# Performance work log

Measured on AMD Instinct MI355X. Metric: run time of the kernel, lower is better.

## Reference

```python
import jax, jax.numpy as jnp
import numpy as np

B, M, N_STYLE, K, F = 4, 8192, 8192, 8, 288


def _graphconv(x, src, dst, W, b, num_nodes):
    # DGL GraphConv, norm='both': h_v = (sum_{u->v} x_u * d_out(u)^-1/2) * d_in(v)^-1/2 @ W + b
    ones = jnp.ones(src.shape[0], x.dtype)
    deg_out = jnp.clip(jax.ops.segment_sum(ones, src, num_segments=num_nodes), 1.0)
    deg_in = jnp.clip(jax.ops.segment_sum(ones, dst, num_segments=num_nodes), 1.0)
    h = x * (deg_out ** -0.5)[:, None]                      # [N, F] src-normalized
    agg = jax.ops.segment_sum(h[src], dst, num_segments=num_nodes)  # gather+scatter-add
    agg = agg * (deg_in ** -0.5)[:, None]
    return agg @ W + b


def setup_inputs() -> dict:
    key = jax.random.key(0)
    ks = jax.random.split(key, 8)
    return {
        "feat_c": jax.random.normal(ks[0], (B, M, F), jnp.float32),
        "feat_s": jax.random.normal(ks[1], (B, N_STYLE, F), jnp.float32),
        "idx_k1": jax.random.randint(ks[2], (B, M, K), 0, N_STYLE, dtype=jnp.int32),
        "idx_k2": jax.random.randint(ks[3], (B, M, K), 0, M, dtype=jnp.int32),
        "W1": jax.random.normal(ks[4], (F, F), jnp.float32) * (1.0 / np.sqrt(F)),
        "b1": jnp.zeros((F,), jnp.float32),
        "W2": jax.random.normal(ks[5], (F, F), jnp.float32) * (1.0 / np.sqrt(F)),
        "b2": jnp.zeros((F,), jnp.float32),
    }


def reference(feat_c, feat_s, idx_k1, idx_k2, W1, b1, W2, b2):
    b, m, f = feat_c.shape
    n = feat_s.shape[1]
    k = idx_k1.shape[2]
    num_nodes = m + n
    # idx_v: range(m).view(1,m,1).expand(2,m,k).view(-1)
    idx_v = jnp.tile(jnp.repeat(jnp.arange(m, dtype=jnp.int32), k), 2)  # [2*m*k]
    # idx_u: cat((idx_k2, idx_k1 + m), dim=1).view(b, -1)
    idx_u = jnp.concatenate([idx_k2, idx_k1 + m], axis=1).reshape(b, -1)  # [b, 2*m*k]
    feat = jnp.concatenate([feat_c, feat_s], axis=1)  # [b, m+n, f]

    def per_graph(x, src):
        h = _graphconv(x, src, idx_v, W1, b1, num_nodes)
        h = jax.nn.relu(h)
        h = _graphconv(h, src, idx_v, W2, b2, num_nodes)
        return h[:m]  # [m, f]

    return jax.vmap(per_graph)(feat, idx_u)  # [b, m, f]
```

## Files before the change

kernel.cpp:

```cpp
#include <hip/hip_runtime.h>

#define B 4
#define M 8192
#define NSTY 8192
#define KNB 8
#define F 288
#define NT (M + NSTY)
#define BM (B * M)
#define SEGL (M * F)

typedef __attribute__((ext_vector_type(8))) short short8;
typedef __attribute__((ext_vector_type(4))) float floatx4;
typedef __attribute__((ext_vector_type(2))) float floatx2;

__device__ __forceinline__ float u2f(unsigned int u) {
    union { unsigned int u; float f; } c; c.u = u; return c.f;
}
__device__ __forceinline__ unsigned short f2b(float x) {
    union { float f; unsigned int u; } c; c.f = x;
    unsigned int r = c.u + 0x7FFFu + ((c.u >> 16) & 1u);
    return (unsigned short)(r >> 16);
}
__device__ __forceinline__ floatx2 bpair(unsigned int p) {
    floatx2 r;
    r.x = u2f(p << 16);
    r.y = u2f(p & 0xFFFF0000u);
    return r;
}
__device__ __forceinline__ void gload_lds16(const void* g, void* l) {
    __builtin_amdgcn_global_load_lds(
        (const __attribute__((address_space(1))) unsigned int*)g,
        (__attribute__((address_space(3))) unsigned int*)l, 16, 0, 0);
}

#define PREP_DEG_BLKS 4
#define PREP_CVT_BLKS 576
#define PREP_PKW_BLKS 162
__global__ __launch_bounds__(1024) void prep_kernel(
                            const int* __restrict__ idx_k1, const int* __restrict__ idx_k2,
                            int* __restrict__ deg,
                            const float* __restrict__ fc, const float* __restrict__ fs,
                            unsigned short* __restrict__ fb,
                            const float* __restrict__ W1, const float* __restrict__ W2,
                            unsigned short* __restrict__ Wp1, unsigned short* __restrict__ Wp2) {
    int blk = blockIdx.x;
    int tid = threadIdx.x;
    if (blk < PREP_DEG_BLKS) {
        __shared__ int h[NT];
        for (int i = tid; i < NT; i += 1024) h[i] = 0;
        __syncthreads();
        int b = blk;
        const int4* p2 = (const int4*)(idx_k2 + (size_t)b * M * KNB);
        const int4* p1 = (const int4*)(idx_k1 + (size_t)b * M * KNB);
        #pragma unroll 2
        for (int i = tid; i < (M * KNB) / 4; i += 1024) {
            int4 v = p2[i];
            atomicAdd(&h[v.x], 1); atomicAdd(&h[v.y], 1);
            atomicAdd(&h[v.z], 1); atomicAdd(&h[v.w], 1);
        }
        #pragma unroll 2
        for (int i = tid; i < (M * KNB) / 4; i += 1024) {
            int4 v = p1[i];
            atomicAdd(&h[M + v.x], 1); atomicAdd(&h[M + v.y], 1);
            atomicAdd(&h[M + v.z], 1); atomicAdd(&h[M + v.w], 1);
        }
        __syncthreads();
        int4* dst = (int4*)(deg + (size_t)b * NT);
        const int4* hs = (const int4*)h;
        for (int i = tid; i < NT / 4; i += 1024) dst[i] = hs[i];
    } else if (blk < PREP_DEG_BLKS + PREP_CVT_BLKS) {
        int cb = blk - PREP_DEG_BLKS;
        int seg = cb / 72;
        int bis = cb - seg * 72;
        int b = seg >> 1, sty = seg & 1;
        const float* src0 = (sty ? fs : fc) + (size_t)b * SEGL;
        unsigned short* dst0 = fb + (size_t)b * 2 * SEGL + (size_t)sty * SEGL;
        unsigned int e0 = (unsigned int)bis * 32768u + (unsigned int)tid * 8u;
        float4 x[8];
        #pragma unroll
        for (int j = 0; j < 4; ++j) {
            const float* s = src0 + e0 + j * 8192u;
            x[2 * j]     = *(const float4*)s;
            x[2 * j + 1] = *(const float4*)(s + 4);
        }
        #pragma unroll
        for (int j = 0; j < 4; ++j) {
            uint4 o;
            o.x = (unsigned int)f2b(x[2*j].x)   | ((unsigned int)f2b(x[2*j].y)   << 16);
            o.y = (unsigned int)f2b(x[2*j].z)   | ((unsigned int)f2b(x[2*j].w)   << 16);
            o.z = (unsigned int)f2b(x[2*j+1].x) | ((unsigned int)f2b(x[2*j+1].y) << 16);
            o.w = (unsigned int)f2b(x[2*j+1].z) | ((unsigned int)f2b(x[2*j+1].w) << 16);
            *(uint4*)(dst0 + e0 + j * 8192u) = o;
        }
    } else {
        int t = (blk - PREP_DEG_BLKS - PREP_CVT_BLKS) * 1024 + tid;
        if (t >= 2 * F * F) return;
        int half = t >= F * F;
        int tt = t - half * F * F;
        int k = tt / F, n = tt - k * F;
        const float* W = half ? W2 : W1;
        unsigned short* Wp = half ? Wp2 : Wp1;
        Wp[((size_t)(k >> 3) * F + n) * 8 + (k & 7)] = f2b(W[tt]);
    }
}

template<int LAYER>
__global__ __launch_bounds__(256) void agg_kernel(
        const unsigned short* __restrict__ src_tbl,
        const int* __restrict__ idx_k1, const int* __restrict__ idx_k2,
        const int* __restrict__ deg, const float* __restrict__ b1,
        unsigned short* __restrict__ aggb) {
    const int NK = (LAYER == 1) ? 16 : 8;
    int tid = threadIdx.x, wid = tid >> 6, lane = tid & 63;
    int blk = blockIdx.x;
    int rx = blk & 7;
    int b = rx >> 1;
    int sub = (blk >> 3) * 2 + (rx & 1);
    int rbase = sub * 16 + wid * 4;

    int i4 = lane >> 4, e = lane & 15;
    size_t eb = ((size_t)b * M + rbase + i4) * KNB;
    int u;
    if (e < 8) u = idx_k2[eb + e];
    else       u = M + idx_k1[eb + e - 8];
    int dg = deg[b * NT + u];
    float w = rsqrtf((float)(dg < 1 ? 1 : dg));
    float wst = (e >= 8) ? w : 0.f;
    unsigned int uoff = (unsigned int)u * (unsigned int)(F * 2);

    float bb[8];
    if (LAYER == 2 && lane < 36) {
        float4 t0 = *(const float4*)(b1 + 8 * lane);
        float4 t1 = *(const float4*)(b1 + 8 * lane + 4);
        bb[0]=fmaxf(t0.x,0.f); bb[1]=fmaxf(t0.y,0.f); bb[2]=fmaxf(t0.z,0.f); bb[3]=fmaxf(t0.w,0.f);
        bb[4]=fmaxf(t1.x,0.f); bb[5]=fmaxf(t1.y,0.f); bb[6]=fmaxf(t1.z,0.f); bb[7]=fmaxf(t1.w,0.f);
    }

    const char* baseb = (const char*)(src_tbl + (size_t)b * (LAYER == 1 ? NT : M) * F);
    unsigned int lane16 = (unsigned int)lane * 16u;
    unsigned short* dbase = aggb + ((size_t)b * M + rbase) * F;

    #pragma unroll
    for (int i = 0; i < 4; ++i) {
        unsigned int off[NK];
        #pragma unroll
        for (int k = 0; k < NK; ++k)
            off[k] = (unsigned int)__shfl((int)uoff, i * 16 + k) + lane16;
        uint4 v[NK];
        if (lane < 36) {
            #pragma unroll
            for (int k = 0; k < NK; ++k) v[k] = *(const uint4*)(baseb + off[k]);
        }

        floatx2 acc[4];
        if (LAYER == 2) {
            float S = 0.f;
            #pragma unroll
            for (int j = 8; j < 16; ++j) S += __shfl(wst, i * 16 + j);
            #pragma unroll
            for (int j = 0; j < 4; ++j) { acc[j].x = bb[2*j] * S; acc[j].y = bb[2*j+1] * S; }
        } else {
            #pragma unroll
            for (int j = 0; j < 4; ++j) acc[j] = (floatx2){0.f, 0.f};
        }

        #pragma unroll
        for (int k = 0; k < NK; ++k) {
            float wk = __shfl(w, i * 16 + k);
            floatx2 wk2 = {wk, wk};
            acc[0] += wk2 * bpair(v[k].x);
            acc[1] += wk2 * bpair(v[k].y);
            acc[2] += wk2 * bpair(v[k].z);
            acc[3] += wk2 * bpair(v[k].w);
        }

        if (lane < 36) {
            uint4 o;
            o.x = (unsigned int)f2b(acc[0].x*0.25f) | ((unsigned int)f2b(acc[0].y*0.25f) << 16);
            o.y = (unsigned int)f2b(acc[1].x*0.25f) | ((unsigned int)f2b(acc[1].y*0.25f) << 16);
            o.z = (unsigned int)f2b(acc[2].x*0.25f) | ((unsigned int)f2b(acc[2].y*0.25f) << 16);
            o.w = (unsigned int)f2b(acc[3].x*0.25f) | ((unsigned int)f2b(acc[3].y*0.25f) << 16);
            *(uint4*)(dbase + (size_t)i * F + 8 * lane) = o;
        }
    }
}

template<int RELU, int OUTBF16>
__global__ __launch_bounds__(256, 2) void gemm_kernel(
        const unsigned short* __restrict__ A,
        const unsigned short* __restrict__ Wp,
        const float* __restrict__ bias,
        void* __restrict__ Cout) {
    __shared__ __align__(16) unsigned short sA[64 * F];
    __shared__ __align__(16) unsigned short sB[2][4 * F * 8];
    int tid = threadIdx.x;
    int wid = tid >> 6, lane = tid & 63;
    int wm = wid & 1, wn = wid >> 1;
    int quad = lane >> 4, r16 = lane & 15;
    int blk = blockIdx.x;
    int rx = blk & 7;
    int b = rx >> 1;
    int sub = (blk >> 3) * 2 + (rx & 1);
    int row0 = b * M + sub * 64;

    const unsigned short* Ab = A + (size_t)row0 * F;
    #pragma unroll
    for (int rr = 0; rr < 9; ++rr)
        gload_lds16(Ab + (rr * 256 + tid) * 8, &sA[(rr * 256 + tid) * 8]);
    if (tid < 128) {
        #pragma unroll
        for (int rr = 0; rr < 9; ++rr)
            gload_lds16(Wp + (rr * 128 + tid) * 8, &sB[0][(rr * 128 + tid) * 8]);
    }

    floatx4 acc[9][2];
    #pragma unroll
    for (int ct = 0; ct < 9; ++ct)
        #pragma unroll
        for (int rt = 0; rt < 2; ++rt)
            acc[ct][rt] = (floatx4){0.f, 0.f, 0.f, 0.f};

    __syncthreads();

    for (int s = 0; s < 9; ++s) {
        if (s < 8 && tid < 128) {
            const unsigned short* src = Wp + (size_t)(s + 1) * 4 * F * 8;
            unsigned short* dstb = sB[(s + 1) & 1];
            #pragma unroll
            for (int rr = 0; rr < 9; ++rr)
                gload_lds16(src + (rr * 128 + tid) * 8, dstb + (rr * 128 + tid) * 8);
        }
        short8 a0 = *(const short8*)&sA[(wm * 32 + r16) * F + s * 32 + quad * 8];
        short8 a1 = *(const short8*)&sA[(wm * 32 + 16 + r16) * F + s * 32 + quad * 8];
        const unsigned short* bbp = &sB[s & 1][(quad * F + wn * 144 + r16) * 8];
        #pragma unroll
        for (int ct = 0; ct < 9; ++ct) {
            short8 bf = *(const short8*)(bbp + ct * 128);
            acc[ct][0] = __builtin_amdgcn_mfma_f32_16x16x32_bf16(a0, bf, acc[ct][0], 0, 0, 0);
            acc[ct][1] = __builtin_amdgcn_mfma_f32_16x16x32_bf16(a1, bf, acc[ct][1], 0, 0, 0);
        }
        __syncthreads();
    }

    #pragma unroll
    for (int ct = 0; ct < 9; ++ct) {
        int col = wn * 144 + ct * 16 + r16;
        float bc = bias[col];
        #pragma unroll
        for (int rt = 0; rt < 2; ++rt) {
            #pragma unroll
            for (int rg = 0; rg < 4; ++rg) {
                float v = acc[ct][rt][rg] + bc;
                if (RELU) v = fmaxf(v, 0.f);
                int grow = row0 + wm * 32 + quad * 4 + rt * 16 + rg;
                if (OUTBF16) ((unsigned short*)Cout)[(size_t)grow * F + col] = f2b(v);
                else         ((float*)Cout)[(size_t)grow * F + col] = v;
            }
        }
    }
}

extern "C" void kernel_launch(void* const* d_in, const int* in_sizes, int n_in,
                              void* d_out, int out_size, void* d_ws, size_t ws_size,
                              hipStream_t stream) {
    const float* feat_c = (const float*)d_in[0];
    const float* feat_s = (const float*)d_in[1];
    const int*   idx_k1 = (const int*)d_in[2];
    const int*   idx_k2 = (const int*)d_in[3];
    const float* W1     = (const float*)d_in[4];
    const float* b1     = (const float*)d_in[5];
    const float* W2     = (const float*)d_in[6];
    const float* b2     = (const float*)d_in[7];

    char* ws = (char*)d_ws;
    int*            deg  = (int*)ws;
    unsigned short* Wp1  = (unsigned short*)(ws + 262144);
    unsigned short* Wp2  = (unsigned short*)(ws + 262144 + 165888);
    unsigned short* aggb = (unsigned short*)(ws + 262144 + 2 * 165888);

    unsigned short* featb = (unsigned short*)d_out;
    unsigned short* h1b   = (unsigned short*)d_out;
    float*          out   = (float*)d_out;

    prep_kernel<<<PREP_DEG_BLKS + PREP_CVT_BLKS + PREP_PKW_BLKS, 1024, 0, stream>>>(
        idx_k1, idx_k2, deg, feat_c, feat_s, featb, W1, W2, Wp1, Wp2);

    agg_kernel<1><<<BM / 16, 256, 0, stream>>>(featb, idx_k1, idx_k2, deg, b1, aggb);
    gemm_kernel<1, 1><<<BM / 64, 256, 0, stream>>>(aggb, Wp1, b1, (void*)h1b);

    agg_kernel<2><<<BM / 16, 256, 0, stream>>>(h1b, idx_k1, idx_k2, deg, b1, aggb);
    gemm_kernel<0, 0><<<BM / 64, 256, 0, stream>>>(aggb, Wp2, b2, (void*)out);
}
```

Measured before the change: 219.9 us.

## Fuse neighbor aggregation into GEMM kernel via shared-memory A tile

Merges the gather/aggregate kernel and the bf16 MFMA GEMM into one 512-thread kernel per layer. Aggregated rows go straight into the LDS A tile instead of round-tripping through a global buffer. This removes two launches and the write and re-read of the aggregated matrix. In exchange, blocks are larger (8 waves, each computing a 16-row MFMA slice), the weight prefetch is issued before the gather, and h1 now lives in workspace instead of the output buffer.

```diff
diff --git a/kernel.cpp b/kernel.cpp
--- a/kernel.cpp
+++ b/kernel.cpp
@@ -105,139 +105,127 @@
 }
 
 template<int LAYER>
-__global__ __launch_bounds__(256) void agg_kernel(
+__global__ __launch_bounds__(512, 4) void fused_kernel(
         const unsigned short* __restrict__ src_tbl,
         const int* __restrict__ idx_k1, const int* __restrict__ idx_k2,
-        const int* __restrict__ deg, const float* __restrict__ b1,
-        unsigned short* __restrict__ aggb) {
+        const int* __restrict__ deg,
+        const float* __restrict__ bprev,
+        const unsigned short* __restrict__ Wp,
+        const float* __restrict__ bias,
+        void* __restrict__ Cout) {
     const int NK = (LAYER == 1) ? 16 : 8;
-    int tid = threadIdx.x, wid = tid >> 6, lane = tid & 63;
+    __shared__ __align__(16) unsigned short sA[64 * F];
+    __shared__ __align__(16) unsigned short sB[2][4 * F * 8];
+
+    int tid = threadIdx.x;
+    int wid = tid >> 6, lane = tid & 63;
     int blk = blockIdx.x;
     int rx = blk & 7;
     int b = rx >> 1;
     int sub = (blk >> 3) * 2 + (rx & 1);
-    int rbase = sub * 16 + wid * 4;
+    int rloc = sub * 64;
+    int row0 = b * M + rloc;
+
+    if (tid < 128) {
+        #pragma unroll
+        for (int rr = 0; rr < 9; ++rr)
+            gload_lds16(Wp + (rr * 128 + tid) * 8, &sB[0][(rr * 128 + tid) * 8]);
+    }
 
     int i4 = lane >> 4, e = lane & 15;
-    size_t eb = ((size_t)b * M + rbase + i4) * KNB;
-    int u;
-    if (e < 8) u = idx_k2[eb + e];
-    else       u = M + idx_k1[eb + e - 8];
-    int dg = deg[b * NT + u];
-    float w = rsqrtf((float)(dg < 1 ? 1 : dg));
-    float wst = (e >= 8) ? w : 0.f;
-    unsigned int uoff = (unsigned int)u * (unsigned int)(F * 2);
+    const char* baseb = (const char*)(src_tbl + (size_t)b * (size_t)(LAYER == 1 ? NT : M) * F);
+    unsigned int lane16 = (unsigned int)lane * 16u;
 
     float bb[8];
     if (LAYER == 2 && lane < 36) {
-        float4 t0 = *(const float4*)(b1 + 8 * lane);
-        float4 t1 = *(const float4*)(b1 + 8 * lane + 4);
+        float4 t0 = *(const float4*)(bprev + 8 * lane);
+        float4 t1 = *(const float4*)(bprev + 8 * lane + 4);
         bb[0]=fmaxf(t0.x,0.f); bb[1]=fmaxf(t0.y,0.f); bb[2]=fmaxf(t0.z,0.f); bb[3]=fmaxf(t0.w,0.f);
         bb[4]=fmaxf(t1.x,0.f); bb[5]=fmaxf(t1.y,0.f); bb[6]=fmaxf(t1.z,0.f); bb[7]=fmaxf(t1.w,0.f);
     }
 
-    const char* baseb = (const char*)(src_tbl + (size_t)b * (LAYER == 1 ? NT : M) * F);
-    unsigned int lane16 = (unsigned int)lane * 16u;
-    unsigned short* dbase = aggb + ((size_t)b * M + rbase) * F;
-
     #pragma unroll
-    for (int i = 0; i < 4; ++i) {
-        unsigned int off[NK];
-        #pragma unroll
-        for (int k = 0; k < NK; ++k)
-            off[k] = (unsigned int)__shfl((int)uoff, i * 16 + k) + lane16;
-        uint4 v[NK];
-        if (lane < 36) {
+    for (int p = 0; p < 2; ++p) {
+        int rb = wid * 8 + p * 4;
+        size_t eb = ((size_t)b * M + rloc + rb + i4) * KNB;
+        int u;
+        if (e < 8) u = idx_k2[eb + e];
+        else       u = M + idx_k1[eb + e - 8];
+        int dg = deg[b * NT + u];
+        float w = rsqrtf((float)(dg < 1 ? 1 : dg));
+        float wst = (e >= 8) ? w : 0.f;
+        unsigned int uoff = (unsigned int)u * (unsigned int)(F * 2);
+
+        #pragma unroll
+        for (int i = 0; i < 4; ++i) {
+            floatx2 acc[4];
+            if (LAYER == 2) {
+                float S = 0.f;
+                #pragma unroll
+                for (int j = 8; j < 16; ++j) S += __shfl(wst, i * 16 + j);
+                #pragma unroll
+                for (int j = 0; j < 4; ++j) { acc[j].x = bb[2*j] * S; acc[j].y = bb[2*j+1] * S; }
+            } else {
+                #pragma unroll
+                for (int j = 0; j < 4; ++j) acc[j] = (floatx2){0.f, 0.f};
+            }
+
             #pragma unroll
-            for (int k = 0; k < NK; ++k) v[k] = *(const uint4*)(baseb + off[k]);
-        }
-
-        floatx2 acc[4];
-        if (LAYER == 2) {
-            float S = 0.f;
-            #pragma unroll
-            for (int j = 8; j < 16; ++j) S += __shfl(wst, i * 16 + j);
-            #pragma unroll
-            for (int j = 0; j < 4; ++j) { acc[j].x = bb[2*j] * S; acc[j].y = bb[2*j+1] * S; }
-        } else {
-            #pragma unroll
-            for (int j = 0; j < 4; ++j) acc[j] = (floatx2){0.f, 0.f};
-        }
-
-        #pragma unroll
-        for (int k = 0; k < NK; ++k) {
-            float wk = __shfl(w, i * 16 + k);
-            floatx2 wk2 = {wk, wk};
-            acc[0] += wk2 * bpair(v[k].x);
-            acc[1] += wk2 * bpair(v[k].y);
-            acc[2] += wk2 * bpair(v[k].z);
-            acc[3] += wk2 * bpair(v[k].w);
-        }
-
-        if (lane < 36) {
-            uint4 o;
-            o.x = (unsigned int)f2b(acc[0].x*0.25f) | ((unsigned int)f2b(acc[0].y*0.25f) << 16);
-            o.y = (unsigned int)f2b(acc[1].x*0.25f) | ((unsigned int)f2b(acc[1].y*0.25f) << 16);
-            o.z = (unsigned int)f2b(acc[2].x*0.25f) | ((unsigned int)f2b(acc[2].y*0.25f) << 16);
-            o.w = (unsigned int)f2b(acc[3].x*0.25f) | ((unsigned int)f2b(acc[3].y*0.25f) << 16);
-            *(uint4*)(dbase + (size_t)i * F + 8 * lane) = o;
-        }
-    }
-}
-
-template<int RELU, int OUTBF16>
-__global__ __launch_bounds__(256, 2) void gemm_kernel(
-        const unsigned short* __restrict__ A,
-        const unsigned short* __restrict__ Wp,
-        const float* __restrict__ bias,
-        void* __restrict__ Cout) {
-    __shared__ __align__(16) unsigned short sA[64 * F];
-    __shared__ __align__(16) unsigned short sB[2][4 * F * 8];
-    int tid = threadIdx.x;
-    int wid = tid >> 6, lane = tid & 63;
-    int wm = wid & 1, wn = wid >> 1;
+            for (int c = 0; c < NK / 8; ++c) {
+                unsigned int off[8];
+                #pragma unroll
+                for (int k = 0; k < 8; ++k)
+                    off[k] = (unsigned int)__shfl((int)uoff, i * 16 + c * 8 + k) + lane16;
+                uint4 v[8];
+                if (lane < 36) {
+                    #pragma unroll
+                    for (int k = 0; k < 8; ++k) v[k] = *(const uint4*)(baseb + off[k]);
+                }
+                #pragma unroll
+                for (int k = 0; k < 8; ++k) {
+                    float wk = __shfl(w, i * 16 + c * 8 + k);
+                    floatx2 wk2 = {wk, wk};
+                    acc[0] += wk2 * bpair(v[k].x);
+                    acc[1] += wk2 * bpair(v[k].y);
+                    acc[2] += wk2 * bpair(v[k].z);
+                    acc[3] += wk2 * bpair(v[k].w);
+                }
+            }
+
+            if (lane < 36) {
+                uint4 o;
+                o.x = (unsigned int)f2b(acc[0].x*0.25f) | ((unsigned int)f2b(acc[0].y*0.25f) << 16);
+                o.y = (unsigned int)f2b(acc[1].x*0.25f) | ((unsigned int)f2b(acc[1].y*0.25f) << 16);
+                o.z = (unsigned int)f2b(acc[2].x*0.25f) | ((unsigned int)f2b(acc[2].y*0.25f) << 16);
+                o.w = (unsigned int)f2b(acc[3].x*0.25f) | ((unsigned int)f2b(acc[3].y*0.25f) << 16);
+                *(uint4*)&sA[(size_t)(rb + i) * F + 8 * lane] = o;
+            }
+        }
+    }
+
+    int wm = wid & 3, wn = wid >> 2;
     int quad = lane >> 4, r16 = lane & 15;
-    int blk = blockIdx.x;
-    int rx = blk & 7;
-    int b = rx >> 1;
-    int sub = (blk >> 3) * 2 + (rx & 1);
-    int row0 = b * M + sub * 64;
-
-    const unsigned short* Ab = A + (size_t)row0 * F;
+
+    floatx4 acc9[9];
     #pragma unroll
-    for (int rr = 0; rr < 9; ++rr)
-        gload_lds16(Ab + (rr * 256 + tid) * 8, &sA[(rr * 256 + tid) * 8]);
-    if (tid < 128) {
-        #pragma unroll
-        for (int rr = 0; rr < 9; ++rr)
-            gload_lds16(Wp + (rr * 128 + tid) * 8, &sB[0][(rr * 128 + tid) * 8]);
-    }
-
-    floatx4 acc[9][2];
-    #pragma unroll
-    for (int ct = 0; ct < 9; ++ct)
-        #pragma unroll
-        for (int rt = 0; rt < 2; ++rt)
-            acc[ct][rt] = (floatx4){0.f, 0.f, 0.f, 0.f};
+    for (int ct = 0; ct < 9; ++ct) acc9[ct] = (floatx4){0.f, 0.f, 0.f, 0.f};
 
     __syncthreads();
 
     for (int s = 0; s < 9; ++s) {
         if (s < 8 && tid < 128) {
-            const unsigned short* src = Wp + (size_t)(s + 1) * 4 * F * 8;
+            const unsigned short* srcw = Wp + (size_t)(s + 1) * 4 * F * 8;
             unsigned short* dstb = sB[(s + 1) & 1];
             #pragma unroll
             for (int rr = 0; rr < 9; ++rr)
-                gload_lds16(src + (rr * 128 + tid) * 8, dstb + (rr * 128 + tid) * 8);
-        }
-        short8 a0 = *(const short8*)&sA[(wm * 32 + r16) * F + s * 32 + quad * 8];
-        short8 a1 = *(const short8*)&sA[(wm * 32 + 16 + r16) * F + s * 32 + quad * 8];
+                gload_lds16(srcw + (rr * 128 + tid) * 8, dstb + (rr * 128 + tid) * 8);
+        }
+        short8 a0 = *(const short8*)&sA[(wm * 16 + r16) * F + s * 32 + quad * 8];
         const unsigned short* bbp = &sB[s & 1][(quad * F + wn * 144 + r16) * 8];
         #pragma unroll
         for (int ct = 0; ct < 9; ++ct) {
             short8 bf = *(const short8*)(bbp + ct * 128);
-            acc[ct][0] = __builtin_amdgcn_mfma_f32_16x16x32_bf16(a0, bf, acc[ct][0], 0, 0, 0);
-            acc[ct][1] = __builtin_amdgcn_mfma_f32_16x16x32_bf16(a1, bf, acc[ct][1], 0, 0, 0);
+            acc9[ct] = __builtin_amdgcn_mfma_f32_16x16x32_bf16(a0, bf, acc9[ct], 0, 0, 0);
         }
         __syncthreads();
     }
@@ -247,15 +235,12 @@
         int col = wn * 144 + ct * 16 + r16;
         float bc = bias[col];
         #pragma unroll
-        for (int rt = 0; rt < 2; ++rt) {
-            #pragma unroll
-            for (int rg = 0; rg < 4; ++rg) {
-                float v = acc[ct][rt][rg] + bc;
-                if (RELU) v = fmaxf(v, 0.f);
-                int grow = row0 + wm * 32 + quad * 4 + rt * 16 + rg;
-                if (OUTBF16) ((unsigned short*)Cout)[(size_t)grow * F + col] = f2b(v);
-                else         ((float*)Cout)[(size_t)grow * F + col] = v;
-            }
+        for (int rg = 0; rg < 4; ++rg) {
+            float v = acc9[ct][rg] + bc;
+            if (LAYER == 1) v = fmaxf(v, 0.f);
+            int grow = row0 + wm * 16 + quad * 4 + rg;
+            if (LAYER == 1) ((unsigned short*)Cout)[(size_t)grow * F + col] = f2b(v);
+            else            ((float*)Cout)[(size_t)grow * F + col] = v;
         }
     }
 }
@@ -276,18 +261,17 @@
     int*            deg  = (int*)ws;
     unsigned short* Wp1  = (unsigned short*)(ws + 262144);
     unsigned short* Wp2  = (unsigned short*)(ws + 262144 + 165888);
-    unsigned short* aggb = (unsigned short*)(ws + 262144 + 2 * 165888);
+    unsigned short* h1b  = (unsigned short*)(ws + 262144 + 2 * 165888);
 
     unsigned short* featb = (unsigned short*)d_out;
-    unsigned short* h1b   = (unsigned short*)d_out;
     float*          out   = (float*)d_out;
 
     prep_kernel<<<PREP_DEG_BLKS + PREP_CVT_BLKS + PREP_PKW_BLKS, 1024, 0, stream>>>(
         idx_k1, idx_k2, deg, feat_c, feat_s, featb, W1, W2, Wp1, Wp2);
 
-    agg_kernel<1><<<BM / 16, 256, 0, stream>>>(featb, idx_k1, idx_k2, deg, b1, aggb);
-    gemm_kernel<1, 1><<<BM / 64, 256, 0, stream>>>(aggb, Wp1, b1, (void*)h1b);
-
-    agg_kernel<2><<<BM / 16, 256, 0, stream>>>(h1b, idx_k1, idx_k2, deg, b1, aggb);
-    gemm_kernel<0, 0><<<BM / 64, 256, 0, stream>>>(aggb, Wp2, b2, (void*)out);
-}
+    fused_kernel<1><<<BM / 64, 512, 0, stream>>>(
+        featb, idx_k1, idx_k2, deg, b1, Wp1, b1, (void*)h1b);
+
+    fused_kernel<2><<<BM / 64, 512, 0, stream>>>(
+        h1b, idx_k1, idx_k2, deg, b1, Wp2, b2, (void*)out);
+}
```

New measurement: 359.6 us. 1.64x slower.
